# Kernel optimization log

Hardware: AMD Instinct MI355X
Metric: run time of the kernel (lower is better)

The kernel has to match this reference:

```python
import jax, jax.numpy as jnp
import numpy as np

N_NODES = 50000
N_EDGES = 800000
D_IN = 64
D_OUT = 64


def setup_inputs() -> dict:
    key = jax.random.key(0)
    k1, k2, k3 = jax.random.split(key, 3)
    x = jax.random.normal(k1, (N_NODES, D_IN), dtype=jnp.float32)
    edge_index = jax.random.randint(k2, (2, N_EDGES), 0, N_NODES, dtype=jnp.int64)
    # xavier_uniform for weight [in, out]
    limit = np.sqrt(6.0 / (D_IN + D_OUT)).astype(np.float32)
    weight = jax.random.uniform(k3, (D_IN, D_OUT), dtype=jnp.float32, minval=-limit, maxval=limit)
    bias = jnp.zeros((D_OUT,), dtype=jnp.float32)
    return {"x": x, "edge_index": edge_index, "weight": weight, "bias": bias}


def reference(x, edge_index, weight, bias):
    n = x.shape[0]
    # add self loops
    loops = jnp.arange(n, dtype=edge_index.dtype)
    row = jnp.concatenate([edge_index[0], loops])  # [E+N]
    col = jnp.concatenate([edge_index[1], loops])  # [E+N]
    # degree over row (as in torch_geometric degree(row, N))
    deg = jax.ops.segment_sum(jnp.ones_like(row, dtype=x.dtype), row, num_segments=n)
    deg_inv_sqrt = jnp.where(deg > 0, jax.lax.rsqrt(deg), jnp.zeros_like(deg))
    norm = deg_inv_sqrt[row] * deg_inv_sqrt[col]  # [E+N]
    h = x @ weight  # [N, D_OUT]
    # gather-scale-scatter: out[col] += h[row] * norm
    out = jax.ops.segment_sum(h[row] * norm[:, None], col, num_segments=n)
    return out + bias
```

## Files before the change

kernel.cpp:

```cpp
#include <hip/hip_runtime.h>
#include <hip/hip_bf16.h>


constexpr int N_NODES = 50000;
constexpr int N_EDGES = 800000;
constexpr int D = 64;
constexpr int NB_SCAN = (N_NODES + 255) / 256;

constexpr int B_SLICE = 64;
constexpr int SLICE = N_EDGES / B_SLICE;
constexpr int PACK8 = N_NODES / 4;
constexpr int QUAR = N_NODES / 4;

static __device__ __forceinline__ unsigned short f2bf(float f) {
    unsigned u = __float_as_uint(f);
    unsigned r = (u + 0x7fffu + ((u >> 16) & 1u)) >> 16;
    return (unsigned short)r;
}
static __device__ __forceinline__ float bf_lo(unsigned v) {
    return __uint_as_float(v << 16);
}
static __device__ __forceinline__ float bf_hi(unsigned v) {
    return __uint_as_float(v & 0xffff0000u);
}

__global__ __launch_bounds__(1024) void hist_priv_kernel(const int* __restrict__ ei,
                                                         unsigned* __restrict__ bh) {
    __shared__ unsigned loc[PACK8];
    int b = blockIdx.x;
    int s = b & (B_SLICE - 1);
    const int* arr = (b < B_SLICE) ? ei : ei + N_EDGES;
    for (int w = threadIdx.x; w < PACK8; w += 1024) loc[w] = 0;
    __syncthreads();
    const int* p = arr + s * SLICE;
    for (int i = threadIdx.x; i < SLICE; i += 1024) {
        int k = p[i];
        atomicAdd(&loc[k >> 2], 1u << (8 * (k & 3)));
    }
    __syncthreads();
    unsigned* dst = bh + (size_t)b * PACK8;
    for (int w = threadIdx.x; w < PACK8; w += 1024) dst[w] = loc[w];
}

__global__ __launch_bounds__(256) void reduce_scan_kernel(const unsigned* __restrict__ bh,
                                                          float* __restrict__ dis,
                                                          int* __restrict__ offs_local,
                                                          int* __restrict__ partials,
                                                          unsigned char* __restrict__ bs8) {
    int t = threadIdx.x;
    int i = blockIdx.x * 256 + t;
    unsigned cl = 0;
    if (i < N_NODES) {
        const int w = i >> 2;
        const unsigned sh = 8 * (i & 3);
        const unsigned* prow = bh + w;
        unsigned dl = 0;
#pragma unroll
        for (int g = 0; g < 4; ++g) {
            unsigned vr[16];
#pragma unroll
            for (int k = 0; k < 16; ++k) vr[k] = prow[(size_t)(g * 16 + k) * PACK8];
#pragma unroll
            for (int k = 0; k < 16; ++k) dl += (vr[k] >> sh) & 0xffu;
        }
        dis[i] = rsqrtf((float)dl + 1.0f);
        const unsigned* pcol = bh + (size_t)B_SLICE * PACK8 + w;
#pragma unroll
        for (int g = 0; g < 4; ++g) {
            unsigned vr[16];
#pragma unroll
            for (int k = 0; k < 16; ++k) vr[k] = pcol[(size_t)(g * 16 + k) * PACK8];
#pragma unroll
            for (int k = 0; k < 16; ++k) {
                bs8[(size_t)(g * 16 + k) * N_NODES + i] = (unsigned char)cl;
                cl += (vr[k] >> sh) & 0xffu;
            }
        }
    }
    __shared__ int s[256];
    s[t] = (int)cl;
    __syncthreads();
    for (int d = 1; d < 256; d <<= 1) {
        int u = (t >= d) ? s[t - d] : 0;
        __syncthreads();
        s[t] += u;
        __syncthreads();
    }
    if (i < N_NODES) offs_local[i] = s[t] - (int)cl;
    if (t == 255) partials[blockIdx.x] = s[t];
}

__global__ __launch_bounds__(256) void offs_kernel(const int* __restrict__ offs_local,
                                                   const int* __restrict__ partials,
                                                   int* __restrict__ offs) {
    __shared__ int pref[256];
    int t = threadIdx.x;
    int v = (t < NB_SCAN) ? partials[t] : 0;
    pref[t] = v;
    __syncthreads();
    for (int d = 1; d < 256; d <<= 1) {
        int u = (t >= d) ? pref[t - d] : 0;
        __syncthreads();
        pref[t] += u;
        __syncthreads();
    }
    int ex = pref[t] - v;
    __syncthreads();
    pref[t] = ex;
    __syncthreads();
    int i = blockIdx.x * 256 + t;
    if (i < N_NODES) offs[i] = pref[blockIdx.x] + offs_local[i];
    if (i == 0) offs[N_NODES] = N_EDGES;
}

__global__ __launch_bounds__(256) void gemm_kernel(const float* __restrict__ x,
                                                   const float* __restrict__ W,
                                                   const float* __restrict__ dis,
                                                   unsigned short* __restrict__ hs) {
    __shared__ float Xs[64][68];
    __shared__ float Ws[64][64];
    int t = threadIdx.x;
    int n0 = blockIdx.x * 64;

    const float4* W4 = (const float4*)W;
    float4* Ws4 = (float4*)Ws;
#pragma unroll
    for (int i = 0; i < 4; ++i) Ws4[t + i * 256] = W4[t + i * 256];

    const float4* x4 = (const float4*)(x + (size_t)n0 * D);
#pragma unroll
    for (int i = 0; i < 4; ++i) {
        int f = t + i * 256;
        int r = f >> 4, c = (f & 15) << 2;
        float4 v = make_float4(0.f, 0.f, 0.f, 0.f);
        if (n0 + r < N_NODES) v = x4[f];
        Xs[r][c] = v.x; Xs[r][c + 1] = v.y; Xs[r][c + 2] = v.z; Xs[r][c + 3] = v.w;
    }
    __syncthreads();

    int tx = t & 15, ty = t >> 4;
    float acc[4][4] = {};
#pragma unroll
    for (int k = 0; k < D; ++k) {
        float a[4], bb[4];
#pragma unroll
        for (int i = 0; i < 4; ++i) a[i] = Xs[ty * 4 + i][k];
#pragma unroll
        for (int jj = 0; jj < 4; ++jj) bb[jj] = Ws[k][tx * 4 + jj];
#pragma unroll
        for (int i = 0; i < 4; ++i)
#pragma unroll
            for (int jj = 0; jj < 4; ++jj)
                acc[i][jj] = fmaf(a[i], bb[jj], acc[i][jj]);
    }

#pragma unroll
    for (int i = 0; i < 4; ++i) {
        int r = ty * 4 + i;
        if (n0 + r < N_NODES) {
            float dr = dis[n0 + r];
            ushort4 v;
            v.x = f2bf(acc[i][0] * dr); v.y = f2bf(acc[i][1] * dr);
            v.z = f2bf(acc[i][2] * dr); v.w = f2bf(acc[i][3] * dr);
            *(ushort4*)(hs + (size_t)(n0 + r) * D + tx * 4) = v;
        }
    }
}

__global__ __launch_bounds__(1024) void bucket_det_kernel(const int* __restrict__ ei,
                                                          const int* __restrict__ offs,
                                                          const unsigned char* __restrict__ bs8,
                                                          int* __restrict__ csr) {
    __shared__ unsigned pos[QUAR];
    const int s = blockIdx.x >> 2;
    const int q = blockIdx.x & 3;
    const int c0 = q * QUAR;
    const int* offq = offs + c0;
    const unsigned char* relq = bs8 + (size_t)s * N_NODES + c0;
    for (int w = threadIdx.x; w < QUAR; w += 1024)
        pos[w] = (unsigned)offq[w] + relq[w];
    __syncthreads();
    const int* rowp = ei + s * SLICE;
    const int* colp = ei + N_EDGES + s * SLICE;
    for (int i = threadIdx.x; i < SLICE; i += 1024) {
        int c = colp[i];
        if (c >= c0 && c < c0 + QUAR) {
            unsigned p = atomicAdd(&pos[c - c0], 1u);
            csr[p] = rowp[i];
        }
    }
}

__global__ __launch_bounds__(256) void gather_kernel(const int* __restrict__ offs,
                                                     const int* __restrict__ csr,
                                                     const unsigned* __restrict__ hs32,
                                                     const float* __restrict__ dis,
                                                     const float* __restrict__ bias,
                                                     float* __restrict__ out) {
    const int wave = threadIdx.x >> 6;
    const int lane = threadIdx.x & 63;
    const int half = lane >> 5;
    const int jj = lane & 31;
    const int n = blockIdx.x * 4 + wave;
    if (n >= N_NODES) return;

    float aLo[4], aHi[4];
#pragma unroll
    for (int k = 0; k < 4; ++k) { aLo[k] = 0.f; aHi[k] = 0.f; }
    {
        unsigned sv = hs32[(size_t)n * 32 + jj];
        if (half == 0) { aLo[0] = bf_lo(sv); aHi[0] = bf_hi(sv); }
    }

    const int beg = __builtin_amdgcn_readfirstlane(offs[n]);
    const int m   = __builtin_amdgcn_readfirstlane(offs[n + 1]) - beg;
    const int* p = csr + beg;

    int i = 0;
    for (; i + 16 <= m; i += 16) {
        int r[8];
#pragma unroll
        for (int k = 0; k < 8; ++k) {
            int rA = p[i + 2 * k];
            int rB = p[i + 2 * k + 1];
            r[k] = half ? rB : rA;
        }
        unsigned v[8];
#pragma unroll
        for (int k = 0; k < 8; ++k) v[k] = hs32[(size_t)r[k] * 32 + jj];
#pragma unroll
        for (int k = 0; k < 8; ++k) {
            aLo[k & 3] += bf_lo(v[k]);
            aHi[k & 3] += bf_hi(v[k]);
        }
    }
    for (; i + 2 <= m; i += 2) {
        int rA = p[i], rB = p[i + 1];
        int r = half ? rB : rA;
        unsigned v = hs32[(size_t)r * 32 + jj];
        aLo[1] += bf_lo(v);
        aHi[1] += bf_hi(v);
    }
    if (i < m) {
        unsigned v = hs32[(size_t)p[i] * 32 + jj];
        if (half == 0) { aLo[2] += bf_lo(v); aHi[2] += bf_hi(v); }
    }

    float tLo = (aLo[0] + aLo[1]) + (aLo[2] + aLo[3]);
    float tHi = (aHi[0] + aHi[1]) + (aHi[2] + aHi[3]);
    tLo += __shfl(tLo, lane ^ 32);
    tHi += __shfl(tHi, lane ^ 32);

    if (half == 0) {
        float dn = dis[n];
        float2 bj = ((const float2*)bias)[jj];
        float2 o;
        o.x = fmaf(dn, tLo, bj.x);
        o.y = fmaf(dn, tHi, bj.y);
        ((float2*)out)[(size_t)n * 32 + jj] = o;
    }
}


__global__ void histf_kernel(const int* __restrict__ row, const int* __restrict__ col,
                             int* __restrict__ degi, int* __restrict__ cnt) {
    int e = blockIdx.x * blockDim.x + threadIdx.x;
    if (e < N_EDGES) {
        atomicAdd(&degi[row[e]], 1);
        atomicAdd(&cnt[col[e]], 1);
    }
}

__global__ void disf_kernel(int* __restrict__ degi) {
    int i = blockIdx.x * blockDim.x + threadIdx.x;
    if (i < N_NODES) {
        float d = (float)degi[i] + 1.0f;
        ((float*)degi)[i] = rsqrtf(d);
    }
}

__global__ void block_scan_kernel(const int* __restrict__ cnt, int* __restrict__ offs,
                                  int* __restrict__ partials) {
    __shared__ int s[256];
    int t = threadIdx.x;
    int i = blockIdx.x * 256 + t;
    int v = (i < N_NODES) ? cnt[i] : 0;
    s[t] = v;
    __syncthreads();
    for (int d = 1; d < 256; d <<= 1) {
        int u = (t >= d) ? s[t - d] : 0;
        __syncthreads();
        s[t] += u;
        __syncthreads();
    }
    if (i < N_NODES) offs[i] = s[t] - v;
    if (t == 255) partials[blockIdx.x] = s[t];
}

__global__ void scan_partials_kernel(int* __restrict__ partials) {
    __shared__ int s[256];
    int t = threadIdx.x;
    int v = (t < NB_SCAN) ? partials[t] : 0;
    s[t] = v;
    __syncthreads();
    for (int d = 1; d < 256; d <<= 1) {
        int u = (t >= d) ? s[t - d] : 0;
        __syncthreads();
        s[t] += u;
        __syncthreads();
    }
    if (t < NB_SCAN) partials[t] = s[t] - v;
}

__global__ void add_off_kernel(int* __restrict__ offs, const int* __restrict__ partials) {
    int i = blockIdx.x * 256 + threadIdx.x;
    if (i < N_NODES) offs[i] += partials[blockIdx.x];
    if (i == 0) offs[N_NODES] = N_EDGES;
}

__global__ void bucket_fb_kernel(const int* __restrict__ row, const int* __restrict__ col,
                                 const int* __restrict__ offs, int* __restrict__ cur,
                                 int* __restrict__ csr) {
    int e = blockIdx.x * blockDim.x + threadIdx.x;
    if (e < N_EDGES) {
        int c = col[e];
        int pos = offs[c] + atomicAdd(&cur[c], 1);
        csr[pos] = row[e];
    }
}


extern "C" void kernel_launch(void* const* d_in, const int* in_sizes, int n_in,
                              void* d_out, int out_size, void* d_ws, size_t ws_size,
                              hipStream_t stream) {
    const float* x    = (const float*)d_in[0];
    const int*   ei   = (const int*)d_in[1];
    const float* W    = (const float*)d_in[2];
    const float* bias = (const float*)d_in[3];
    float* out = (float*)d_out;

    char* ws = (char*)d_ws;
    float*          dis      = (float*)(ws + 0);
    int*            offs     = (int*)(ws + 200000);
    int*            offs_loc = (int*)(ws + 400064);
    int*            cur      = (int*)(ws + 600064);
    int*            partials = (int*)(ws + 800064);
    int*            csr      = (int*)(ws + 801088);
    unsigned short* hs       = (unsigned short*)(ws + 4001088);
    unsigned*       bh       = (unsigned*)(ws + 10401088);
    unsigned char*  bs8      = (unsigned char*)(ws + 16801088);

    const size_t WS_NEEDED = 20001088;

    if (ws_size >= WS_NEEDED) {
        hist_priv_kernel<<<2 * B_SLICE, 1024, 0, stream>>>(ei, bh);
        reduce_scan_kernel<<<NB_SCAN, 256, 0, stream>>>(bh, dis, offs_loc, partials, bs8);
        offs_kernel<<<NB_SCAN, 256, 0, stream>>>(offs_loc, partials, offs);
        gemm_kernel<<<(N_NODES + 63) / 64, 256, 0, stream>>>(x, W, dis, hs);
        bucket_det_kernel<<<4 * B_SLICE, 1024, 0, stream>>>(ei, offs, bs8, csr);
        gather_kernel<<<(N_NODES + 3) / 4, 256, 0, stream>>>(offs, csr, (const unsigned*)hs,
                                                             dis, bias, out);
    } else {
        const int* row = ei;
        const int* col = ei + N_EDGES;
        int* degi = (int*)dis;
        int* cntf = offs_loc;
        hipMemsetAsync(ws, 0, 800064, stream);
        histf_kernel<<<(N_EDGES + 255) / 256, 256, 0, stream>>>(row, col, degi, cntf);
        disf_kernel<<<(N_NODES + 255) / 256, 256, 0, stream>>>(degi);
        block_scan_kernel<<<NB_SCAN, 256, 0, stream>>>(cntf, offs, partials);
        scan_partials_kernel<<<1, 256, 0, stream>>>(partials);
        add_off_kernel<<<NB_SCAN, 256, 0, stream>>>(offs, partials);
        gemm_kernel<<<(N_NODES + 63) / 64, 256, 0, stream>>>(x, W, dis, hs);
        bucket_fb_kernel<<<(N_EDGES + 255) / 256, 256, 0, stream>>>(row, col, offs, cur, csr);
        gather_kernel<<<(N_NODES + 3) / 4, 256, 0, stream>>>(offs, csr, (const unsigned*)hs,
                                                             dis, bias, out);
    }
}
```

Baseline: 152.2 us.

## Switch gather to one bf16 feature per lane and tune gemm unrolling

The gather kernel drops the split-wave scheme, where each lane loaded a packed pair of bf16 values and two half-waves handled alternate edges. Each of the 64 lanes now loads one bf16 feature per edge, 16 edges are unrolled per step, and the half-wave shuffle reduction is gone. This gives simpler indexing and more loads in flight, but each lane issues narrower 2-byte loads and the number of load instructions per edge doubles. The gemm kernel also gets an occupancy hint in its launch bounds and a partial unroll of the k loop, which should lower register pressure.

```diff
diff --git a/kernel.cpp b/kernel.cpp
--- a/kernel.cpp
+++ b/kernel.cpp
@@ -17,11 +17,8 @@
     unsigned r = (u + 0x7fffu + ((u >> 16) & 1u)) >> 16;
     return (unsigned short)r;
 }
-static __device__ __forceinline__ float bf_lo(unsigned v) {
-    return __uint_as_float(v << 16);
-}
-static __device__ __forceinline__ float bf_hi(unsigned v) {
-    return __uint_as_float(v & 0xffff0000u);
+static __device__ __forceinline__ float bf2f(unsigned short s) {
+    return __uint_as_float((unsigned)s << 16);
 }
 
 __global__ __launch_bounds__(1024) void hist_priv_kernel(const int* __restrict__ ei,
@@ -113,10 +110,10 @@
     if (i == 0) offs[N_NODES] = N_EDGES;
 }
 
-__global__ __launch_bounds__(256) void gemm_kernel(const float* __restrict__ x,
-                                                   const float* __restrict__ W,
-                                                   const float* __restrict__ dis,
-                                                   unsigned short* __restrict__ hs) {
+__global__ __launch_bounds__(256, 4) void gemm_kernel(const float* __restrict__ x,
+                                                      const float* __restrict__ W,
+                                                      const float* __restrict__ dis,
+                                                      unsigned short* __restrict__ hs) {
     __shared__ float Xs[64][68];
     __shared__ float Ws[64][64];
     int t = threadIdx.x;
@@ -140,7 +137,7 @@
 
     int tx = t & 15, ty = t >> 4;
     float acc[4][4] = {};
-#pragma unroll
+#pragma unroll 8
     for (int k = 0; k < D; ++k) {
         float a[4], bb[4];
 #pragma unroll
@@ -193,72 +190,45 @@
 
 __global__ __launch_bounds__(256) void gather_kernel(const int* __restrict__ offs,
                                                      const int* __restrict__ csr,
-                                                     const unsigned* __restrict__ hs32,
+                                                     const unsigned short* __restrict__ hs,
                                                      const float* __restrict__ dis,
                                                      const float* __restrict__ bias,
                                                      float* __restrict__ out) {
-    const int wave = threadIdx.x >> 6;
-    const int lane = threadIdx.x & 63;
-    const int half = lane >> 5;
-    const int jj = lane & 31;
-    const int n = blockIdx.x * 4 + wave;
+    int wave = threadIdx.x >> 6;
+    int j = threadIdx.x & 63;
+    int n = blockIdx.x * 4 + wave;
     if (n >= N_NODES) return;
 
-    float aLo[4], aHi[4];
-#pragma unroll
-    for (int k = 0; k < 4; ++k) { aLo[k] = 0.f; aHi[k] = 0.f; }
-    {
-        unsigned sv = hs32[(size_t)n * 32 + jj];
-        if (half == 0) { aLo[0] = bf_lo(sv); aHi[0] = bf_hi(sv); }
-    }
-
-    const int beg = __builtin_amdgcn_readfirstlane(offs[n]);
-    const int m   = __builtin_amdgcn_readfirstlane(offs[n + 1]) - beg;
+    float a[8];
+    a[0] = bf2f(hs[(size_t)n * D + j]);
+#pragma unroll
+    for (int k = 1; k < 8; ++k) a[k] = 0.f;
+
+    int beg = __builtin_amdgcn_readfirstlane(offs[n]);
+    int m   = __builtin_amdgcn_readfirstlane(offs[n + 1]) - beg;
     const int* p = csr + beg;
 
     int i = 0;
     for (; i + 16 <= m; i += 16) {
-        int r[8];
-#pragma unroll
-        for (int k = 0; k < 8; ++k) {
-            int rA = p[i + 2 * k];
-            int rB = p[i + 2 * k + 1];
-            r[k] = half ? rB : rA;
-        }
-        unsigned v[8];
-#pragma unroll
-        for (int k = 0; k < 8; ++k) v[k] = hs32[(size_t)r[k] * 32 + jj];
-#pragma unroll
-        for (int k = 0; k < 8; ++k) {
-            aLo[k & 3] += bf_lo(v[k]);
-            aHi[k & 3] += bf_hi(v[k]);
-        }
-    }
-    for (; i + 2 <= m; i += 2) {
-        int rA = p[i], rB = p[i + 1];
-        int r = half ? rB : rA;
-        unsigned v = hs32[(size_t)r * 32 + jj];
-        aLo[1] += bf_lo(v);
-        aHi[1] += bf_hi(v);
-    }
-    if (i < m) {
-        unsigned v = hs32[(size_t)p[i] * 32 + jj];
-        if (half == 0) { aLo[2] += bf_lo(v); aHi[2] += bf_hi(v); }
-    }
-
-    float tLo = (aLo[0] + aLo[1]) + (aLo[2] + aLo[3]);
-    float tHi = (aHi[0] + aHi[1]) + (aHi[2] + aHi[3]);
-    tLo += __shfl(tLo, lane ^ 32);
-    tHi += __shfl(tHi, lane ^ 32);
-
-    if (half == 0) {
-        float dn = dis[n];
-        float2 bj = ((const float2*)bias)[jj];
-        float2 o;
-        o.x = fmaf(dn, tLo, bj.x);
-        o.y = fmaf(dn, tHi, bj.y);
-        ((float2*)out)[(size_t)n * 32 + jj] = o;
-    }
+        int r[16];
+        float v[16];
+#pragma unroll
+        for (int k = 0; k < 16; ++k) r[k] = p[i + k];
+#pragma unroll
+        for (int k = 0; k < 16; ++k) v[k] = bf2f(hs[(size_t)r[k] * D + j]);
+#pragma unroll
+        for (int k = 0; k < 16; ++k) a[k & 7] += v[k];
+    }
+    for (; i + 4 <= m; i += 4) {
+        int r0 = p[i], r1 = p[i + 1], r2 = p[i + 2], r3 = p[i + 3];
+        a[0] += bf2f(hs[(size_t)r0 * D + j]);
+        a[1] += bf2f(hs[(size_t)r1 * D + j]);
+        a[2] += bf2f(hs[(size_t)r2 * D + j]);
+        a[3] += bf2f(hs[(size_t)r3 * D + j]);
+    }
+    for (; i < m; ++i) a[1] += bf2f(hs[(size_t)p[i] * D + j]);
+    float tot = ((a[0] + a[1]) + (a[2] + a[3])) + ((a[4] + a[5]) + (a[6] + a[7]));
+    out[(size_t)n * D + j] = fmaf(dis[n], tot, bias[j]);
 }
 
 
@@ -358,8 +328,7 @@
         offs_kernel<<<NB_SCAN, 256, 0, stream>>>(offs_loc, partials, offs);
         gemm_kernel<<<(N_NODES + 63) / 64, 256, 0, stream>>>(x, W, dis, hs);
         bucket_det_kernel<<<4 * B_SLICE, 1024, 0, stream>>>(ei, offs, bs8, csr);
-        gather_kernel<<<(N_NODES + 3) / 4, 256, 0, stream>>>(offs, csr, (const unsigned*)hs,
-                                                             dis, bias, out);
+        gather_kernel<<<(N_NODES + 3) / 4, 256, 0, stream>>>(offs, csr, hs, dis, bias, out);
     } else {
         const int* row = ei;
         const int* col = ei + N_EDGES;
@@ -373,7 +342,6 @@
         add_off_kernel<<<NB_SCAN, 256, 0, stream>>>(offs, partials);
         gemm_kernel<<<(N_NODES + 63) / 64, 256, 0, stream>>>(x, W, dis, hs);
         bucket_fb_kernel<<<(N_EDGES + 255) / 256, 256, 0, stream>>>(row, col, offs, cur, csr);
-        gather_kernel<<<(N_NODES + 3) / 4, 256, 0, stream>>>(offs, csr, (const unsigned*)hs,
-                                                             dis, bias, out);
-    }
-}
+        gather_kernel<<<(N_NODES + 3) / 4, 256, 0, stream>>>(offs, csr, hs, dis, bias, out);
+    }
+}
```

Measured after the change: 133.7 us. 12.1% less time.
